# Kernel optimization log

Hardware: AMD Instinct MI355X
Metric: run time of the kernel (lower is better)

## Reference

```python
import jax, jax.numpy as jnp
import numpy as np

HEADS = 8
MODEL_DIM = 64
EPS = 1e-5


def _layernorm(x, gamma, beta):
    mu = jnp.mean(x, axis=-1, keepdims=True)
    var = jnp.var(x, axis=-1, keepdims=True)
    return (x - mu) * jax.lax.rsqrt(var + EPS) * gamma + beta


def setup_inputs() -> dict:
    key = jax.random.key(0)
    ks = jax.random.split(key, 5)
    bs, h, w, in_dim = 8, 32, 32, 512
    hd = HEADS * MODEL_DIM  # 512
    s = 0.02
    return {
        "x": jax.random.normal(ks[0], (bs, h, w, in_dim), jnp.float32),
        "Wq": jax.random.normal(ks[1], (in_dim, hd), jnp.float32) * s,
        "Wk": jax.random.normal(ks[2], (in_dim, hd), jnp.float32) * s,
        "Wv": jax.random.normal(ks[3], (in_dim, hd), jnp.float32) * s,
        "Wo": jax.random.normal(ks[4], (hd, in_dim), jnp.float32) * s,
        "gamma": jnp.ones((in_dim,), jnp.float32),
        "beta": jnp.zeros((in_dim,), jnp.float32),
    }


def reference(x, Wq, Wk, Wv, Wo, gamma, beta):
    bs, h, w, in_dim = x.shape
    # pre_norm=True: normalize first; residual uses the normalized x (as in original)
    xn = _layernorm(x, gamma, beta)
    Q = (xn @ Wq).reshape(bs, h, w, HEADS, MODEL_DIM)
    K = (xn @ Wk).reshape(bs, h, w, HEADS, MODEL_DIM)
    V = (xn @ Wv).reshape(bs, h, w, HEADS, MODEL_DIM)
    # full (h,w) x (h,w) correlation per head
    corr = jnp.einsum('bijhd,bklhd->bijhkl', Q, K) / jnp.sqrt(
        jnp.asarray(MODEL_DIM, x.dtype))
    cshape = corr.shape
    attn = jax.nn.softmax(corr.reshape(*cshape[:-2], -1), axis=-1).reshape(cshape)
    logits = jnp.einsum('bijhkl,bklhd->bijhd', attn, V).reshape(bs, h, w, -1)
    out = logits @ Wo + xn
    return out, attn
```

## Files before the change

### kernel.cpp

```cpp
#include <hip/hip_runtime.h>
#include <hip/hip_bf16.h>

typedef __attribute__((ext_vector_type(8))) short bf16x8;
typedef __attribute__((ext_vector_type(4))) short s16x4;
typedef __attribute__((ext_vector_type(4))) float f32x4;

#define DIM 512
#define NH 8
#define HD 64
#define SEQ 1024
#define NB 8
#define ROWS (NB*SEQ)

__device__ __forceinline__ short f2bf(float f) {
  union { float f; unsigned u; } v; v.f = f;
  unsigned r = v.u + 0x7fffu + ((v.u >> 16) & 1u);
  return (short)(r >> 16);
}
__device__ __forceinline__ float bf2f(short s) {
  union { unsigned u; float f; } v; v.u = ((unsigned)(unsigned short)s) << 16;
  return v.f;
}
__device__ __forceinline__ f32x4 mfma16(bf16x8 a, bf16x8 b, f32x4 c) {
  return __builtin_amdgcn_mfma_f32_16x16x32_bf16(a, b, c, 0, 0, 0);
}
__device__ __forceinline__ void gload16(const void* g, void* l) {
  __builtin_amdgcn_global_load_lds(
      (const __attribute__((address_space(1))) unsigned int*)g,
      (__attribute__((address_space(3))) unsigned int*)l, 16, 0, 0);
}
__device__ __forceinline__ void lds_barrier() {
  __builtin_amdgcn_sched_barrier(0);
  asm volatile("s_waitcnt lgkmcnt(0)" ::: "memory");
  __builtin_amdgcn_s_barrier();
  __builtin_amdgcn_sched_barrier(0);
}

__global__ __launch_bounds__(256) void ln_kernel(const float* __restrict__ x,
    const float* __restrict__ gamma, const float* __restrict__ beta,
    short* __restrict__ xnb) {
  const int t = threadIdx.x;
  const int row = blockIdx.x * 4 + (t >> 6);
  const int lane = t & 63;
  const float4* xr = reinterpret_cast<const float4*>(x + (size_t)row * DIM);
  const float4 a = xr[lane * 2], b2 = xr[lane * 2 + 1];
  float s = a.x + a.y + a.z + a.w + b2.x + b2.y + b2.z + b2.w;
  float sq = a.x*a.x + a.y*a.y + a.z*a.z + a.w*a.w +
             b2.x*b2.x + b2.y*b2.y + b2.z*b2.z + b2.w*b2.w;
  for (int off = 1; off < 64; off <<= 1) {
    s += __shfl_xor(s, off);
    sq += __shfl_xor(sq, off);
  }
  const float mean = s * (1.0f / DIM);
  const float var = sq * (1.0f / DIM) - mean * mean;
  const float rs = rsqrtf(var + 1e-5f);
  const float4 ga = reinterpret_cast<const float4*>(gamma)[lane * 2];
  const float4 gb = reinterpret_cast<const float4*>(gamma)[lane * 2 + 1];
  const float4 ba = reinterpret_cast<const float4*>(beta)[lane * 2];
  const float4 bb = reinterpret_cast<const float4*>(beta)[lane * 2 + 1];
  union { bf16x8 v; short sh[8]; } o;
  o.sh[0] = f2bf((a.x - mean) * rs * ga.x + ba.x);
  o.sh[1] = f2bf((a.y - mean) * rs * ga.y + ba.y);
  o.sh[2] = f2bf((a.z - mean) * rs * ga.z + ba.z);
  o.sh[3] = f2bf((a.w - mean) * rs * ga.w + ba.w);
  o.sh[4] = f2bf((b2.x - mean) * rs * gb.x + bb.x);
  o.sh[5] = f2bf((b2.y - mean) * rs * gb.y + bb.y);
  o.sh[6] = f2bf((b2.z - mean) * rs * gb.z + bb.z);
  o.sh[7] = f2bf((b2.w - mean) * rs * gb.w + bb.w);
  *reinterpret_cast<bf16x8*>(xnb + (size_t)row * DIM + lane * 8) = o.v;
}

__global__ __launch_bounds__(256) void wtrans_kernel(
    const float* __restrict__ Wq, const float* __restrict__ Wk,
    const float* __restrict__ Wv, const float* __restrict__ Wo,
    short* __restrict__ WqkvT, short* __restrict__ WoT) {
  __shared__ float tl[64 * 65];
  const int y = blockIdx.y;
  const float* W = (y == 0) ? Wq : (y == 1) ? Wk : (y == 2) ? Wv : Wo;
  const int tile = blockIdx.x;
  const int k0 = (tile >> 3) * 64, n0 = (tile & 7) * 64;
  const int t = threadIdx.x;
#pragma unroll
  for (int i = 0; i < 16; ++i) {
    const int idx = i * 256 + t;
    const int k = idx >> 6, n = idx & 63;
    tl[n * 65 + k] = W[(size_t)(k0 + k) * 512 + n0 + n];
  }
  __syncthreads();
#pragma unroll
  for (int i = 0; i < 16; ++i) {
    const int idx = i * 256 + t;
    const int n = idx >> 6, k = idx & 63;
    const short v = f2bf(tl[n * 65 + k]);
    if (y < 3) WqkvT[(size_t)(y * 512 + n0 + n) * 512 + k0 + k] = v;
    else       WoT[(size_t)(n0 + n) * 512 + k0 + k] = v;
  }
}

#define GEMM_MAIN(A_, BT_, m0_, n0_)                                          \
  f32x4 acc[4][4] = {};                                                       \
  {                                                                           \
    const int srow_a = w * 32 + (lane >> 2);                                  \
    const int key_a = (srow_a ^ (srow_a >> 2)) & 3;                           \
    const int sseg = (lane & 3) ^ key_a;                                      \
    const short* ga0 = A_ + (size_t)(m0_ + srow_a) * 512 + 8 * sseg;          \
    const short* ga1 = A_ + (size_t)(m0_ + srow_a + 16) * 512 + 8 * ((lane & 3) ^ (((srow_a + 16) ^ ((srow_a + 16) >> 2)) & 3)); \
    const short* gb0 = BT_ + (size_t)(n0_ + srow_a) * 512 + 8 * sseg;         \
    const short* gb1 = BT_ + (size_t)(n0_ + srow_a + 16) * 512 + 8 * ((lane & 3) ^ (((srow_a + 16) ^ ((srow_a + 16) >> 2)) & 3)); \
    for (int kb = 0; kb < 512; kb += 32) {                                    \
      __syncthreads();                                                        \
      gload16(ga0 + kb, &As[(w * 2 + 0) * 512]);                              \
      gload16(ga1 + kb, &As[(w * 2 + 1) * 512]);                              \
      gload16(gb0 + kb, &Bs[(w * 2 + 0) * 512]);                              \
      gload16(gb1 + kb, &Bs[(w * 2 + 1) * 512]);                              \
      __syncthreads();                                                        \
      bf16x8 af[4], bf[4];                                                    \
      _Pragma("unroll")                                                       \
      for (int i = 0; i < 4; ++i) {                                           \
        const int ra = 64 * wr + 16 * i + c16;                                \
        af[i] = *reinterpret_cast<const bf16x8*>(                             \
            &As[ra * 32 + 8 * (g ^ ((ra ^ (ra >> 2)) & 3))]);                 \
        const int rb = 64 * wc + 16 * i + c16;                                \
        bf[i] = *reinterpret_cast<const bf16x8*>(                             \
            &Bs[rb * 32 + 8 * (g ^ ((rb ^ (rb >> 2)) & 3))]);                 \
      }                                                                       \
      _Pragma("unroll")                                                       \
      for (int i = 0; i < 4; ++i)                                             \
        _Pragma("unroll")                                                     \
        for (int j = 0; j < 4; ++j)                                           \
          acc[i][j] = mfma16(af[i], bf[j], acc[i][j]);                        \
    }                                                                         \
  }

__global__ __launch_bounds__(256) void gemm_qkv(const short* __restrict__ A,
    const short* __restrict__ BT, short* __restrict__ Qo,
    short* __restrict__ Ko, short* __restrict__ Vt) {
  __shared__ short As[128 * 32];
  __shared__ short Bs[128 * 32];
  const int m0 = blockIdx.x * 128, n0 = blockIdx.y * 128;
  const int t = threadIdx.x, w = t >> 6, lane = t & 63, g = lane >> 4, c16 = lane & 15;
  const int wr = w >> 1, wc = w & 1;
  GEMM_MAIN(A, BT, m0, n0)
  const int z = n0 >> 9;
  const int nl = n0 & 511;
#pragma unroll
  for (int i = 0; i < 4; ++i)
#pragma unroll
    for (int j = 0; j < 4; ++j)
#pragma unroll
      for (int e = 0; e < 4; ++e) {
        const int row = m0 + 64 * wr + 16 * i + 4 * g + e;
        const int col = nl + 64 * wc + 16 * j + c16;
        const short v = f2bf(acc[i][j][e]);
        if (z == 0) {
          Qo[(size_t)row * 512 + col] = v;
        } else if (z == 1) {
          Ko[(size_t)row * 512 + col] = v;
        } else {
          const int bb = row >> 10, ss = row & 1023, hh = col >> 6, dd = col & 63;
          Vt[((size_t)(bb * NH + hh)) * 65536 + dd * 1024 + ss] = v;
        }
      }
}

__global__ __launch_bounds__(256) void gemm_out(const short* __restrict__ A,
    const short* __restrict__ BT, const short* __restrict__ xnb,
    float* __restrict__ out) {
  __shared__ short As[128 * 32];
  __shared__ short Bs[128 * 32];
  const int m0 = blockIdx.x * 128, n0 = blockIdx.y * 128;
  const int t = threadIdx.x, w = t >> 6, lane = t & 63, g = lane >> 4, c16 = lane & 15;
  const int wr = w >> 1, wc = w & 1;
  GEMM_MAIN(A, BT, m0, n0)
#pragma unroll
  for (int i = 0; i < 4; ++i)
#pragma unroll
    for (int j = 0; j < 4; ++j)
#pragma unroll
      for (int e = 0; e < 4; ++e) {
        const int row = m0 + 64 * wr + 16 * i + 4 * g + e;
        const int col = n0 + 64 * wc + 16 * j + c16;
        const size_t idx = (size_t)row * 512 + col;
        out[idx] = acc[i][j][e] + bf2f(xnb[idx]);
      }
}

__global__ __launch_bounds__(256) void attn_kernel(
    const short* __restrict__ Qb, const short* __restrict__ Kb,
    const short* __restrict__ Vt, float* __restrict__ attnOut,
    short* __restrict__ Lg) {
  const int bid = blockIdx.x;
  const int rb = (bid >> 3) & 63;
  const int inst = (bid & 7) * 8 + (bid >> 9);
  const int b = inst >> 3, h = inst & 7;
  const int t = threadIdx.x;
  const int w = t >> 6, lane = t & 63, g = lane >> 4, c16 = lane & 15;
  const int rl = lane >> 3, sgl = lane & 7;

  __shared__ __align__(16) char smem[32768];
  __shared__ float red[2][4][16];
  short* Klds = (short*)smem;
  float* P32 = (float*)smem;
  short* P16 = (short*)(smem + 8448);
  short* Vl  = (short*)(smem + 12800);

  const short* qp = Qb + ((size_t)(b * SEQ + rb * 16 + c16)) * DIM + h * HD + 8 * g;
  const bf16x8 qf0 = *reinterpret_cast<const bf16x8*>(qp);
  const bf16x8 qf1 = *reinterpret_cast<const bf16x8*>(qp + 32);

  const short* kgbase = Kb + ((size_t)b * SEQ) * DIM + h * HD;
  const int swz = 8 * (sgl ^ rl);

#define KSTAGE(c_, buf_)                                                       \
  do {                                                                         \
    __builtin_amdgcn_sched_barrier(0);                                         \
    _Pragma("unroll") for (int i_ = 0; i_ < 4; ++i_) {                         \
      gload16(kgbase + (size_t)((c_) * 128 + 32 * w + 8 * i_ + rl) * DIM + swz,\
              &Klds[(buf_) * 8192 + (32 * w + 8 * i_) * 64]);                  \
    }                                                                          \
  } while (0)

  KSTAGE(0, 0);
  f32x4 acc[16] = {};
  const int sw = c16 & 7;
#pragma unroll
  for (int c = 0; c < 8; ++c) {
    if (c < 7) KSTAGE(c + 1, (c + 1) & 1);
    if (c < 7) { asm volatile("s_waitcnt vmcnt(4)" ::: "memory"); }
    else       { asm volatile("s_waitcnt vmcnt(0)" ::: "memory"); }
    __builtin_amdgcn_sched_barrier(0);
    const short* kl = &Klds[(c & 1) * 8192];
#pragma unroll
    for (int j = 0; j < 2; ++j) {
      const int lr = 32 * w + 16 * j + c16;
      bf16x8 k0 = *reinterpret_cast<const bf16x8*>(&kl[lr * 64 + 8 * (g ^ sw)]);
      bf16x8 k1 = *reinterpret_cast<const bf16x8*>(&kl[lr * 64 + 8 * ((g + 4) ^ sw)]);
      const int tt = c * 2 + j;
      acc[tt] = mfma16(k0, qf0, acc[tt]);
      acc[tt] = mfma16(k1, qf1, acc[tt]);
    }
  }

  const short* vgbase = Vt + (size_t)inst * 65536;
  const int vd = t >> 4, vseg = t & 15;
  bf16x8 vreg[4];
#pragma unroll
  for (int it = 0; it < 4; ++it)
    vreg[it] = *reinterpret_cast<const bf16x8*>(
        vgbase + (size_t)(vd + 16 * it) * 1024 + vseg * 8);

  float m = -1e30f;
#pragma unroll
  for (int tt = 0; tt < 16; ++tt)
#pragma unroll
    for (int e = 0; e < 4; ++e) {
      acc[tt][e] *= 0.125f;
      m = fmaxf(m, acc[tt][e]);
    }
  m = fmaxf(m, __shfl_xor(m, 16));
  m = fmaxf(m, __shfl_xor(m, 32));
  if (g == 0) red[0][w][c16] = m;
  lds_barrier();
  m = fmaxf(fmaxf(red[0][0][c16], red[0][1][c16]),
            fmaxf(red[0][2][c16], red[0][3][c16]));
  float sm = 0.f;
#pragma unroll
  for (int tt = 0; tt < 16; ++tt)
#pragma unroll
    for (int e = 0; e < 4; ++e) {
      const float p = __expf(acc[tt][e] - m);
      acc[tt][e] = p;
      sm += p;
    }
  sm += __shfl_xor(sm, 16);
  sm += __shfl_xor(sm, 32);
  if (g == 0) red[1][w][c16] = sm;
  lds_barrier();
  const float rinv = 1.0f / (red[1][0][c16] + red[1][1][c16] +
                             red[1][2][c16] + red[1][3][c16]);

  f32x4 pacc[4] = {};
  const int qrow = t >> 4, qs = t & 15;
  float* abase2 = attnOut + (size_t)b * 8388608 +
                  (size_t)(rb * 16 + qrow) * 8192 + h * 1024;
#pragma unroll
  for (int c = 0; c < 8; ++c) {
    lds_barrier();
#pragma unroll
    for (int it = 0; it < 4; ++it)
      *reinterpret_cast<bf16x8*>(&Vl[(vd + 16 * it) * 136 + vseg * 8]) = vreg[it];
#pragma unroll
    for (int j = 0; j < 2; ++j) {
      const int col = 32 * w + 16 * j + 4 * g;
      f32x4 pv;
#pragma unroll
      for (int e = 0; e < 4; ++e) pv[e] = acc[2 * c + j][e] * rinv;
      *reinterpret_cast<f32x4*>(&P32[c16 * 132 + col]) = pv;
      s16x4 pb;
#pragma unroll
      for (int e = 0; e < 4; ++e) pb[e] = f2bf(pv[e]);
      *reinterpret_cast<s16x4*>(&P16[c16 * 136 + col]) = pb;
    }
    if (c < 7) {
#pragma unroll
      for (int it = 0; it < 4; ++it)
        vreg[it] = *reinterpret_cast<const bf16x8*>(
            vgbase + (size_t)(vd + 16 * it) * 1024 + (c + 1) * 128 + vseg * 8);
    }
    lds_barrier();
    {
      float* arow = abase2 + c * 128;
      const f32x4 s0 = *reinterpret_cast<const f32x4*>(&P32[qrow * 132 + 4 * qs]);
      const f32x4 s1 = *reinterpret_cast<const f32x4*>(&P32[qrow * 132 + 64 + 4 * qs]);
      __builtin_nontemporal_store(s0, reinterpret_cast<f32x4*>(arow + 4 * qs));
      __builtin_nontemporal_store(s1, reinterpret_cast<f32x4*>(arow + 64 + 4 * qs));
    }
    {
      const bf16x8 pa = *reinterpret_cast<const bf16x8*>(
          &P16[c16 * 136 + 32 * w + 8 * g]);
#pragma unroll
      for (int dt = 0; dt < 4; ++dt) {
        const bf16x8 vb = *reinterpret_cast<const bf16x8*>(
            &Vl[(16 * dt + c16) * 136 + 32 * w + 8 * g]);
        pacc[dt] = mfma16(pa, vb, pacc[dt]);
      }
    }
  }

  lds_barrier();
  f32x4* red2 = reinterpret_cast<f32x4*>(smem);
#pragma unroll
  for (int dt = 0; dt < 4; ++dt) red2[(w * 4 + dt) * 64 + lane] = pacc[dt];
  lds_barrier();
  {
    const int dt = w;
    f32x4 s = red2[dt * 64 + lane];
#pragma unroll
    for (int w2 = 1; w2 < 4; ++w2) {
      f32x4 o = red2[(w2 * 4 + dt) * 64 + lane];
#pragma unroll
      for (int e = 0; e < 4; ++e) s[e] += o[e];
    }
    short* lrow = Lg + ((size_t)(b * SEQ + rb * 16 + 4 * g)) * DIM + h * HD + 16 * dt + c16;
#pragma unroll
    for (int e = 0; e < 4; ++e) lrow[(size_t)e * DIM] = f2bf(s[e]);
  }
}

extern "C" void kernel_launch(void* const* d_in, const int* in_sizes, int n_in,
                              void* d_out, int out_size, void* d_ws, size_t ws_size,
                              hipStream_t stream) {
  const float* x = (const float*)d_in[0];
  const float* Wq = (const float*)d_in[1];
  const float* Wk = (const float*)d_in[2];
  const float* Wv = (const float*)d_in[3];
  const float* Wo = (const float*)d_in[4];
  const float* gamma = (const float*)d_in[5];
  const float* beta = (const float*)d_in[6];
  float* out = (float*)d_out;
  float* attn = out + (size_t)ROWS * DIM;

  char* ws = (char*)d_ws;
  short* xnb = (short*)ws;
  short* WqkvT = (short*)(ws + (size_t)8 * 1024 * 1024);
  short* WoT = WqkvT + 1536 * 512;
  short* Qb = (short*)(ws + (size_t)10 * 1024 * 1024);
  short* Kbp = (short*)(ws + (size_t)18 * 1024 * 1024);
  short* Vt = (short*)(ws + (size_t)26 * 1024 * 1024);
  short* Lg = (short*)(ws + (size_t)34 * 1024 * 1024);

  ln_kernel<<<2048, 256, 0, stream>>>(x, gamma, beta, xnb);
  wtrans_kernel<<<dim3(64, 4), 256, 0, stream>>>(Wq, Wk, Wv, Wo, WqkvT, WoT);
  gemm_qkv<<<dim3(64, 12), 256, 0, stream>>>(xnb, WqkvT, Qb, Kbp, Vt);
  attn_kernel<<<4096, 256, 0, stream>>>(Qb, Kbp, Vt, attn, Lg);
  gemm_out<<<dim3(64, 4), 256, 0, stream>>>(Lg, WoT, xnb, out);
}
```

Baseline: 143.3 us.

## Pre-swizzle V into MFMA fragment layout and deepen GEMM K-tile to 64

Result: faster. 139.5 us (-2.7%).

```diff
diff --git a/kernel.cpp b/kernel.cpp
--- a/kernel.cpp
+++ b/kernel.cpp
@@ -97,50 +97,53 @@
   }
 }
 
-#define GEMM_MAIN(A_, BT_, m0_, n0_)                                          \
+#define GEMM64_MAIN(A_, BT_, m0_, n0_)                                        \
   f32x4 acc[4][4] = {};                                                       \
   {                                                                           \
-    const int srow_a = w * 32 + (lane >> 2);                                  \
-    const int key_a = (srow_a ^ (srow_a >> 2)) & 3;                           \
-    const int sseg = (lane & 3) ^ key_a;                                      \
-    const short* ga0 = A_ + (size_t)(m0_ + srow_a) * 512 + 8 * sseg;          \
-    const short* ga1 = A_ + (size_t)(m0_ + srow_a + 16) * 512 + 8 * ((lane & 3) ^ (((srow_a + 16) ^ ((srow_a + 16) >> 2)) & 3)); \
-    const short* gb0 = BT_ + (size_t)(n0_ + srow_a) * 512 + 8 * sseg;         \
-    const short* gb1 = BT_ + (size_t)(n0_ + srow_a + 16) * 512 + 8 * ((lane & 3) ^ (((srow_a + 16) ^ ((srow_a + 16) >> 2)) & 3)); \
-    for (int kb = 0; kb < 512; kb += 32) {                                    \
+    const int srow = 8 * w + (lane >> 3);                                     \
+    const int sseg = lane & 7;                                                \
+    for (int kb = 0; kb < 512; kb += 64) {                                    \
       __syncthreads();                                                        \
-      gload16(ga0 + kb, &As[(w * 2 + 0) * 512]);                              \
-      gload16(ga1 + kb, &As[(w * 2 + 1) * 512]);                              \
-      gload16(gb0 + kb, &Bs[(w * 2 + 0) * 512]);                              \
-      gload16(gb1 + kb, &Bs[(w * 2 + 1) * 512]);                              \
+      _Pragma("unroll")                                                       \
+      for (int p = 0; p < 4; ++p) {                                           \
+        const int r = 32 * p + srow;                                          \
+        const int gs = 8 * (sseg ^ (r & 7));                                  \
+        gload16(A_ + (size_t)(m0_ + r) * 512 + kb + gs,                       \
+                &As[(32 * p + 8 * w) * 64]);                                  \
+        gload16(BT_ + (size_t)(n0_ + r) * 512 + kb + gs,                      \
+                &Bs[(32 * p + 8 * w) * 64]);                                  \
+      }                                                                       \
       __syncthreads();                                                        \
-      bf16x8 af[4], bf[4];                                                    \
       _Pragma("unroll")                                                       \
-      for (int i = 0; i < 4; ++i) {                                           \
-        const int ra = 64 * wr + 16 * i + c16;                                \
-        af[i] = *reinterpret_cast<const bf16x8*>(                             \
-            &As[ra * 32 + 8 * (g ^ ((ra ^ (ra >> 2)) & 3))]);                 \
-        const int rb = 64 * wc + 16 * i + c16;                                \
-        bf[i] = *reinterpret_cast<const bf16x8*>(                             \
-            &Bs[rb * 32 + 8 * (g ^ ((rb ^ (rb >> 2)) & 3))]);                 \
+      for (int half = 0; half < 2; ++half) {                                  \
+        bf16x8 af[4], bfr[4];                                                 \
+        _Pragma("unroll")                                                     \
+        for (int i = 0; i < 4; ++i) {                                         \
+          const int ra = 64 * wr + 16 * i + c16;                              \
+          af[i] = *reinterpret_cast<const bf16x8*>(                           \
+              &As[ra * 64 + 8 * ((4 * half + g) ^ (ra & 7))]);                \
+          const int rb = 64 * wc + 16 * i + c16;                              \
+          bfr[i] = *reinterpret_cast<const bf16x8*>(                          \
+              &Bs[rb * 64 + 8 * ((4 * half + g) ^ (rb & 7))]);                \
+        }                                                                     \
+        _Pragma("unroll")                                                     \
+        for (int i = 0; i < 4; ++i)                                           \
+          _Pragma("unroll")                                                   \
+          for (int j = 0; j < 4; ++j)                                         \
+            acc[i][j] = mfma16(af[i], bfr[j], acc[i][j]);                     \
       }                                                                       \
-      _Pragma("unroll")                                                       \
-      for (int i = 0; i < 4; ++i)                                             \
-        _Pragma("unroll")                                                     \
-        for (int j = 0; j < 4; ++j)                                           \
-          acc[i][j] = mfma16(af[i], bf[j], acc[i][j]);                        \
     }                                                                         \
   }
 
 __global__ __launch_bounds__(256) void gemm_qkv(const short* __restrict__ A,
     const short* __restrict__ BT, short* __restrict__ Qo,
-    short* __restrict__ Ko, short* __restrict__ Vt) {
-  __shared__ short As[128 * 32];
-  __shared__ short Bs[128 * 32];
+    short* __restrict__ Ko, short* __restrict__ VtF) {
+  __shared__ short As[128 * 64];
+  __shared__ short Bs[128 * 64];
   const int m0 = blockIdx.x * 128, n0 = blockIdx.y * 128;
   const int t = threadIdx.x, w = t >> 6, lane = t & 63, g = lane >> 4, c16 = lane & 15;
   const int wr = w >> 1, wc = w & 1;
-  GEMM_MAIN(A, BT, m0, n0)
+  GEMM64_MAIN(A, BT, m0, n0)
   const int z = n0 >> 9;
   const int nl = n0 & 511;
 #pragma unroll
@@ -158,7 +161,11 @@
           Ko[(size_t)row * 512 + col] = v;
         } else {
           const int bb = row >> 10, ss = row & 1023, hh = col >> 6, dd = col & 63;
-          Vt[((size_t)(bb * NH + hh)) * 65536 + dd * 1024 + ss] = v;
+          const int cch = ss >> 7, kk = ss & 127;
+          const int w2 = kk >> 5, g2 = (kk >> 3) & 3, ee = kk & 7;
+          const int dt2 = dd >> 4, c162 = dd & 15;
+          VtF[((size_t)((((bb * NH + hh) * 8 + cch) * 4 + w2) * 4 + dt2) << 9) +
+              (g2 * 16 + c162) * 8 + ee] = v;
         }
       }
 }
@@ -166,12 +173,12 @@
 __global__ __launch_bounds__(256) void gemm_out(const short* __restrict__ A,
     const short* __restrict__ BT, const short* __restrict__ xnb,
     float* __restrict__ out) {
-  __shared__ short As[128 * 32];
-  __shared__ short Bs[128 * 32];
+  __shared__ short As[128 * 64];
+  __shared__ short Bs[128 * 64];
   const int m0 = blockIdx.x * 128, n0 = blockIdx.y * 128;
   const int t = threadIdx.x, w = t >> 6, lane = t & 63, g = lane >> 4, c16 = lane & 15;
   const int wr = w >> 1, wc = w & 1;
-  GEMM_MAIN(A, BT, m0, n0)
+  GEMM64_MAIN(A, BT, m0, n0)
 #pragma unroll
   for (int i = 0; i < 4; ++i)
 #pragma unroll
@@ -187,7 +194,7 @@
 
 __global__ __launch_bounds__(256) void attn_kernel(
     const short* __restrict__ Qb, const short* __restrict__ Kb,
-    const short* __restrict__ Vt, float* __restrict__ attnOut,
+    const short* __restrict__ VtF, float* __restrict__ attnOut,
     short* __restrict__ Lg) {
   const int bid = blockIdx.x;
   const int rb = (bid >> 3) & 63;
@@ -200,9 +207,9 @@
   __shared__ __align__(16) char smem[32768];
   __shared__ float red[2][4][16];
   short* Klds = (short*)smem;
-  float* P32 = (float*)smem;
-  short* P16 = (short*)(smem + 8448);
-  short* Vl  = (short*)(smem + 12800);
+  float* P32a = (float*)smem;
+  float* P32b = (float*)(smem + 8448);
+  short* P16 = (short*)(smem + 16896);
 
   const short* qp = Qb + ((size_t)(b * SEQ + rb * 16 + c16)) * DIM + h * HD + 8 * g;
   const bf16x8 qf0 = *reinterpret_cast<const bf16x8*>(qp);
@@ -241,13 +248,11 @@
     }
   }
 
-  const short* vgbase = Vt + (size_t)inst * 65536;
-  const int vd = t >> 4, vseg = t & 15;
+  const short* vf = VtF + (size_t)inst * 65536;
   bf16x8 vreg[4];
 #pragma unroll
-  for (int it = 0; it < 4; ++it)
-    vreg[it] = *reinterpret_cast<const bf16x8*>(
-        vgbase + (size_t)(vd + 16 * it) * 1024 + vseg * 8);
+  for (int dt = 0; dt < 4; ++dt)
+    vreg[dt] = *reinterpret_cast<const bf16x8*>(vf + (size_t)((w * 4 + dt) * 512) + lane * 8);
 
   float m = -1e30f;
 #pragma unroll
@@ -285,45 +290,40 @@
                   (size_t)(rb * 16 + qrow) * 8192 + h * 1024;
 #pragma unroll
   for (int c = 0; c < 8; ++c) {
-    lds_barrier();
-#pragma unroll
-    for (int it = 0; it < 4; ++it)
-      *reinterpret_cast<bf16x8*>(&Vl[(vd + 16 * it) * 136 + vseg * 8]) = vreg[it];
+    float* P32w = (c & 1) ? P32b : P32a;
 #pragma unroll
     for (int j = 0; j < 2; ++j) {
       const int col = 32 * w + 16 * j + 4 * g;
       f32x4 pv;
 #pragma unroll
       for (int e = 0; e < 4; ++e) pv[e] = acc[2 * c + j][e] * rinv;
-      *reinterpret_cast<f32x4*>(&P32[c16 * 132 + col]) = pv;
+      *reinterpret_cast<f32x4*>(&P32w[c16 * 132 + col]) = pv;
       s16x4 pb;
 #pragma unroll
       for (int e = 0; e < 4; ++e) pb[e] = f2bf(pv[e]);
       *reinterpret_cast<s16x4*>(&P16[c16 * 136 + col]) = pb;
     }
+    {
+      const bf16x8 pa = *reinterpret_cast<const bf16x8*>(
+          &P16[c16 * 136 + 32 * w + 8 * g]);
+#pragma unroll
+      for (int dt = 0; dt < 4; ++dt)
+        pacc[dt] = mfma16(pa, vreg[dt], pacc[dt]);
+    }
     if (c < 7) {
 #pragma unroll
-      for (int it = 0; it < 4; ++it)
-        vreg[it] = *reinterpret_cast<const bf16x8*>(
-            vgbase + (size_t)(vd + 16 * it) * 1024 + (c + 1) * 128 + vseg * 8);
+      for (int dt = 0; dt < 4; ++dt)
+        vreg[dt] = *reinterpret_cast<const bf16x8*>(
+            vf + (size_t)((((c + 1) * 4 + w) * 4 + dt) * 512) + lane * 8);
     }
     lds_barrier();
     {
       float* arow = abase2 + c * 128;
-      const f32x4 s0 = *reinterpret_cast<const f32x4*>(&P32[qrow * 132 + 4 * qs]);
-      const f32x4 s1 = *reinterpret_cast<const f32x4*>(&P32[qrow * 132 + 64 + 4 * qs]);
+      const float* P32r = (c & 1) ? P32b : P32a;
+      const f32x4 s0 = *reinterpret_cast<const f32x4*>(&P32r[qrow * 132 + 4 * qs]);
+      const f32x4 s1 = *reinterpret_cast<const f32x4*>(&P32r[qrow * 132 + 64 + 4 * qs]);
       __builtin_nontemporal_store(s0, reinterpret_cast<f32x4*>(arow + 4 * qs));
       __builtin_nontemporal_store(s1, reinterpret_cast<f32x4*>(arow + 64 + 4 * qs));
-    }
-    {
-      const bf16x8 pa = *reinterpret_cast<const bf16x8*>(
-          &P16[c16 * 136 + 32 * w + 8 * g]);
-#pragma unroll
-      for (int dt = 0; dt < 4; ++dt) {
-        const bf16x8 vb = *reinterpret_cast<const bf16x8*>(
-            &Vl[(16 * dt + c16) * 136 + 32 * w + 8 * g]);
-        pacc[dt] = mfma16(pa, vb, pacc[dt]);
-      }
     }
   }
 
@@ -366,12 +366,12 @@
   short* WoT = WqkvT + 1536 * 512;
   short* Qb = (short*)(ws + (size_t)10 * 1024 * 1024);
   short* Kbp = (short*)(ws + (size_t)18 * 1024 * 1024);
-  short* Vt = (short*)(ws + (size_t)26 * 1024 * 1024);
+  short* VtF = (short*)(ws + (size_t)26 * 1024 * 1024);
   short* Lg = (short*)(ws + (size_t)34 * 1024 * 1024);
 
   ln_kernel<<<2048, 256, 0, stream>>>(x, gamma, beta, xnb);
   wtrans_kernel<<<dim3(64, 4), 256, 0, stream>>>(Wq, Wk, Wv, Wo, WqkvT, WoT);
-  gemm_qkv<<<dim3(64, 12), 256, 0, stream>>>(xnb, WqkvT, Qb, Kbp, Vt);
-  attn_kernel<<<4096, 256, 0, stream>>>(Qb, Kbp, Vt, attn, Lg);
+  gemm_qkv<<<dim3(64, 12), 256, 0, stream>>>(xnb, WqkvT, Qb, Kbp, VtF);
+  attn_kernel<<<4096, 256, 0, stream>>>(Qb, Kbp, VtF, attn, Lg);
   gemm_out<<<dim3(64, 4), 256, 0, stream>>>(Lg, WoT, xnb, out);
 }
```
